# Optimization experiments

Measured on AMD Instinct MI355X. Metric: run time of the kernel, lower is better.

The kernel has to match this reference:

```python
import jax, jax.numpy as jnp
import numpy as np

MODEL_DIM = 1024
N_Q_HEADS = 16
N_GROUPS = 4
KV_PER_Q = N_Q_HEADS // N_GROUPS        # 4
HEAD_DIM = MODEL_DIM // N_Q_HEADS       # 64
KV_HEAD_DIM = MODEL_DIM // KV_PER_Q     # 256 (per-group K/V total width = N_GROUPS*HEAD_DIM)
ROPE_THETA = 50000.0


def rope_cos_sin(seq_len, dim, dtype):
    # standard RoPE tables: [S, dim]
    inv_freq = 1.0 / (ROPE_THETA ** (jnp.arange(0, dim, 2, dtype=jnp.float32) / dim))
    freqs = jnp.arange(seq_len, dtype=jnp.float32)[:, None] * inv_freq[None, :]  # [S, dim/2]
    emb = jnp.concatenate([freqs, freqs], axis=-1)                               # [S, dim]
    return jnp.cos(emb).astype(dtype), jnp.sin(emb).astype(dtype)


def rotate_half(x):
    h = x.shape[-1] // 2
    return jnp.concatenate([-x[..., h:], x[..., :h]], axis=-1)


def setup_inputs() -> dict:
    key = jax.random.key(0)
    k0, k1, k2, k3, k4 = jax.random.split(key, 5)
    B, S = 2, 2048
    qkv_out = MODEL_DIM + 2 * KV_HEAD_DIM  # 1536
    s_in = 1.0 / np.sqrt(MODEL_DIM)
    return {
        "x": jax.random.normal(k0, (B, S, MODEL_DIM), jnp.float32),
        "W_qkv": jax.random.normal(k1, (MODEL_DIM, qkv_out), jnp.float32) * s_in,
        "b_qkv": jnp.zeros((qkv_out,), jnp.float32),
        "W_out": jax.random.normal(k2, (MODEL_DIM, MODEL_DIM), jnp.float32) * s_in,
        "b_out": jnp.zeros((MODEL_DIM,), jnp.float32),
    }


def reference(x, W_qkv, b_qkv, W_out, b_out):
    B, S, _ = x.shape
    fused = x @ W_qkv + b_qkv  # [B,S,MODEL_DIM + 2*KV_HEAD_DIM]
    q, k, v = jnp.split(fused, [MODEL_DIM, MODEL_DIM + KV_HEAD_DIM], axis=-1)

    # [B,S,(NH HD)] -> [B,NH,S,HD]
    q = q.reshape(B, S, N_Q_HEADS, HEAD_DIM).transpose(0, 2, 1, 3)
    k = k.reshape(B, S, N_GROUPS, HEAD_DIM).transpose(0, 2, 1, 3)
    v = v.reshape(B, S, N_GROUPS, HEAD_DIM).transpose(0, 2, 1, 3)

    cos, sin = rope_cos_sin(S, HEAD_DIM, x.dtype)  # [S,HD]
    cos = cos[None, None]                          # [1,1,S,HD]
    sin = sin[None, None]
    q = q * cos + rotate_half(q) * sin
    k = k * cos + rotate_half(k) * sin

    # GQA without materializing duplicated heads: group queries [B,G,R,S,HD]
    qg = q.reshape(B, N_GROUPS, KV_PER_Q, S, HEAD_DIM)
    scale = 1.0 / np.sqrt(HEAD_DIM)
    scores = jnp.einsum('bgrsh,bgth->bgrst', qg, k) * scale  # [B,G,R,S,S]
    causal = jnp.tril(jnp.ones((S, S), bool))
    scores = jnp.where(causal, scores, jnp.finfo(scores.dtype).min)
    probs = jax.nn.softmax(scores, axis=-1)
    out = jnp.einsum('bgrst,bgth->bgrsh', probs, v)          # [B,G,R,S,HD]

    # [B,G,R,S,HD] -> [B,S,MODEL_DIM]  (head index = g*R + r, matching duplicate_heads)
    out = out.reshape(B, N_Q_HEADS, S, HEAD_DIM).transpose(0, 2, 1, 3).reshape(B, S, MODEL_DIM)
    return out @ W_out + b_out
```

## Files before the change

### kernel.cpp

```cpp
#include <hip/hip_runtime.h>
#include <hip/hip_bf16.h>

typedef __attribute__((ext_vector_type(8))) short short8;
typedef __attribute__((ext_vector_type(4))) float f32x4;

__device__ __forceinline__ short tobf(float f) {
  __hip_bfloat16 h = __float2bfloat16(f);
  return *reinterpret_cast<short*>(&h);
}
__device__ __forceinline__ float frombf(short s) {
  unsigned u = ((unsigned)(unsigned short)s) << 16;
  return __uint_as_float(u);
}

__device__ __forceinline__ int swz(int row) { return (row ^ (row >> 3)) & 7; }

#define GLDS16(gp, lp) __builtin_amdgcn_global_load_lds( \
    (__attribute__((address_space(1))) void*)(gp),       \
    (__attribute__((address_space(3))) void*)(lp), 16, 0, 0)

#define QSCALE 0.18033688011112042f

__global__ __launch_bounds__(256) void prep_k(
    const float* __restrict__ x, short* __restrict__ xb,
    const float* __restrict__ Wqkv, short* __restrict__ WqkvT,
    const float* __restrict__ Wout, short* __restrict__ WoutT,
    float* __restrict__ cost, float* __restrict__ sint) {
  __shared__ float t[64][65];
  const int bx = blockIdx.x, tid = threadIdx.x;
  if (bx < 1024) {
    int base = bx * 4096 + tid * 4;
#pragma unroll
    for (int rep = 0; rep < 4; ++rep) {
      int i = base + rep * 1024;
      float4 v = *(const float4*)(x + i);
      *(short4*)(xb + i) = make_short4(tobf(v.x), tobf(v.y), tobf(v.z), tobf(v.w));
    }
  } else if (bx < 1664) {
    const float* in;
    short* out;
    int C, bb;
    if (bx < 1408) { in = Wqkv; out = WqkvT; C = 1536; bb = bx - 1024; }
    else           { in = Wout; out = WoutT; C = 1024; bb = bx - 1408; }
    const int R = 1024;
    int nc = C >> 6;
    int br = bb / nc, bc = bb % nc;
    int lr = tid >> 6, lc = tid & 63;
#pragma unroll
    for (int j = 0; j < 16; ++j) {
      int r = j * 4 + lr;
      t[r][lc] = in[(size_t)(br * 64 + r) * C + bc * 64 + lc];
    }
    __syncthreads();
#pragma unroll
    for (int j = 0; j < 16; ++j) {
      int r = j * 4 + lr;
      out[(size_t)(bc * 64 + r) * R + br * 64 + lc] = tobf(t[lc][r]);
    }
  } else {
    int t2 = (bx - 1664) * 256 + tid;
    int s = t2 >> 5, f = t2 & 31;
    float inv = __expf(-(float)f * (logf(50000.0f) / 32.0f));
    float a = (float)s * inv;
    cost[t2] = cosf(a);
    sint[t2] = sinf(a);
  }
}

template <int MODE>
__global__ __launch_bounds__(256) void gemm_k(
    const short* __restrict__ A, const short* __restrict__ Bt,
    const float* __restrict__ bias, void* __restrict__ Cout,
    short* __restrict__ vT,
    int M, int N, int K,
    const float* __restrict__ cost, const float* __restrict__ sint) {
  __shared__ short As[128 * 64];
  __shared__ short Bs[64 * 64];
  const int ntile = N >> 6;
  const int bm = blockIdx.x / ntile, bn = blockIdx.x % ntile;
  const int tid = threadIdx.x, w = tid >> 6, l = tid & 63;
  const int c = l & 15, g = l >> 4;
  const int m0 = bm * 128, n0 = bn * 64;

  f32x4 acc[2][4] = {};

  for (int k0 = 0; k0 < K; k0 += 64) {
#pragma unroll
    for (int j = 0; j < 4; ++j) {
      int rb = j * 32 + w * 8;
      int row = rb + (l >> 3);
      int colel = ((l & 7) ^ swz(row)) * 8;
      GLDS16(A + (size_t)(m0 + row) * K + k0 + colel, &As[rb * 64]);
      if (j < 2) GLDS16(Bt + (size_t)(n0 + row) * K + k0 + colel, &Bs[rb * 64]);
    }
    __syncthreads();
#pragma unroll
    for (int kk = 0; kk < 2; ++kk) {
      short8 af[2], bf[4];
#pragma unroll
      for (int mi = 0; mi < 2; ++mi) {
        int row = w * 32 + mi * 16 + c;
        af[mi] = *(const short8*)&As[row * 64 + ((kk * 4 + g) ^ swz(row)) * 8];
      }
#pragma unroll
      for (int ni = 0; ni < 4; ++ni) {
        int row = ni * 16 + c;
        bf[ni] = *(const short8*)&Bs[row * 64 + ((kk * 4 + g) ^ swz(row)) * 8];
      }
#pragma unroll
      for (int mi = 0; mi < 2; ++mi)
#pragma unroll
        for (int ni = 0; ni < 4; ++ni)
          acc[mi][ni] = __builtin_amdgcn_mfma_f32_16x16x32_bf16(af[mi], bf[ni], acc[mi][ni], 0, 0, 0);
    }
    __syncthreads();
  }

  if (MODE == 0 && n0 >= 1280) {
    const int hg = (n0 - 1280) >> 6;
#pragma unroll
    for (int mi = 0; mi < 2; ++mi) {
      int m0r = m0 + w * 32 + mi * 16 + g * 4;
      int b = m0r >> 11, s = m0r & 2047;
#pragma unroll
      for (int ni = 0; ni < 4; ++ni) {
        int d = ni * 16 + c;
        float bs = bias[n0 + d];
        short4 o;
        o.x = tobf(acc[mi][ni][0] + bs);
        o.y = tobf(acc[mi][ni][1] + bs);
        o.z = tobf(acc[mi][ni][2] + bs);
        o.w = tobf(acc[mi][ni][3] + bs);
        *(short4*)&vT[(size_t)((b * 4 + hg) * 64 + d) * 2048 + s] = o;
      }
    }
    return;
  }

#pragma unroll
  for (int mi = 0; mi < 2; ++mi)
#pragma unroll
    for (int r = 0; r < 4; ++r) {
      int m = m0 + w * 32 + mi * 16 + g * 4 + r;
      int s = m & 2047;
#pragma unroll
      for (int ni = 0; ni < 4; ++ni) {
        int n = n0 + ni * 16 + c;
        float v = acc[mi][ni][r] + bias[n];
        if (MODE == 0) {
          int d = n & 63, f = d & 31;
          float cs = cost[s * 32 + f], sn = sint[s * 32 + f];
          float partner = acc[mi][ni ^ 2][r] + bias[n ^ 32];
          v = (d < 32) ? (v * cs - partner * sn) : (v * cs + partner * sn);
          if (n < 1024) v *= QSCALE;
          ((short*)Cout)[(size_t)m * N + n] = tobf(v);
        } else {
          ((float*)Cout)[(size_t)m * N + n] = v;
        }
      }
    }
}

__global__ __launch_bounds__(256) void attn_k(const short* __restrict__ qkv,
                                              const short* __restrict__ vT,
                                              short* __restrict__ pacc,
                                              float* __restrict__ plrun) {
  __shared__ short Ks2[2][64 * 64];
  __shared__ short Vt2[2][64 * 64];
  __shared__ short Ps[4][16 * 64];

  const int bx = blockIdx.x;
  const int bh = bx & 31;
  const int rest = bx >> 5;
  const int p = rest & 7;
  const int ci = rest >> 3;
  const int qtB = 15 - p, qtA = p;
  const int sB = 32 - 2 * p;
  const int start = (ci < 2) ? ci * 9 : 18 + (ci - 2) * 8;
  const int end = (ci < 2) ? start + 9 : start + 8;
  const int b = bh >> 4, h = bh & 15, hg = h >> 2;
  const int tid = threadIdx.x, w = tid >> 6, l = tid & 63;
  const int c = l & 15, g = l >> 4;
  const size_t rowbase = (size_t)(b * 2048) * 1536;

  const int i0row = w * 16 + (l >> 3);
  const int i1row = w * 16 + 8 + (l >> 3);
  const int c0 = ((l & 7) ^ swz(i0row)) * 8;
  const int c1 = ((l & 7) ^ swz(i1row)) * 8;
  const size_t k0off = (size_t)i0row * 1536 + c0;
  const size_t k1off = (size_t)i1row * 1536 + c1;
  const size_t v0off = (size_t)i0row * 2048 + c0;
  const size_t v1off = (size_t)i1row * 2048 + c1;
  const int lds0 = (w * 16) * 64;
  const int lds1 = (w * 16 + 8) * 64;
  const short* kbase = qkv + rowbase + 1024 + hg * 64;
  const short* vbase_p = vT + (size_t)((b * 4 + hg) * 64) * 2048;

#define KTOF(i) (((i) < sB) ? (i) : ((i) - sB))

  {
    int kt0 = KTOF(start);
    GLDS16(kbase + (size_t)kt0 * 98304 + k0off, &Ks2[0][lds0]);
    GLDS16(kbase + (size_t)kt0 * 98304 + k1off, &Ks2[0][lds1]);
    GLDS16(vbase_p + kt0 * 64 + v0off, &Vt2[0][lds0]);
    GLDS16(vbase_p + kt0 * 64 + v1off, &Vt2[0][lds1]);
  }
  asm volatile("s_waitcnt vmcnt(0)" ::: "memory");
  __builtin_amdgcn_s_barrier();
  __builtin_amdgcn_sched_barrier(0);

  f32x4 acco[2][4] = {};
  float lrun[2] = {0.f, 0.f};
  short* Pw = &Ps[w][0];
  short8 aq[2][2];

#pragma unroll
  for (int set = 0; set < 2; ++set)
#pragma unroll
    for (int kk = 0; kk < 2; ++kk)
      aq[set][kk] = *(const short8*)(qkv + rowbase +
          (size_t)(qtB * 128 + w * 32 + set * 16 + c) * 1536 + h * 64 + kk * 32 + g * 8);

#define BODY(qtc)                                                               \
  {                                                                             \
    const int cur = (i - start) & 1, nxt = cur ^ 1;                             \
    const int kt = KTOF(i);                                                     \
    if (i + 1 < end) {                         \
      int kt2 = KTOF(i + 1);                                                    \
      GLDS16(kbase + (size_t)kt2 * 98304 + k0off, &Ks2[nxt][lds0]);             \
      GLDS16(kbase + (size_t)kt2 * 98304 + k1off, &Ks2[nxt][lds1]);             \
      GLDS16(vbase_p + kt2 * 64 + v0off, &Vt2[nxt][lds0]);                      \
      GLDS16(vbase_p + kt2 * 64 + v1off, &Vt2[nxt][lds1]);                      \
    }                                                                           \
    short8 bk[2][4];                                                            \
    _Pragma("unroll") for (int kk = 0; kk < 2; ++kk)                            \
      _Pragma("unroll") for (int nb = 0; nb < 4; ++nb) {                        \
        int row = nb * 16 + c;                                                  \
        bk[kk][nb] = *(const short8*)&Ks2[cur][row * 64 + ((kk * 4 + g) ^ swz(row)) * 8]; \
      }                                                                         \
    f32x4 sfr[2][4] = {};                                                       \
    __builtin_amdgcn_s_setprio(1);                                              \
    _Pragma("unroll") for (int set = 0; set < 2; ++set)                         \
      _Pragma("unroll") for (int kk = 0; kk < 2; ++kk)                          \
        _Pragma("unroll") for (int nb = 0; nb < 4; ++nb)                        \
          sfr[set][nb] = __builtin_amdgcn_mfma_f32_16x16x32_bf16(               \
              bk[kk][nb], aq[set][kk], sfr[set][nb], 0, 0, 0);                  \
    __builtin_amdgcn_s_setprio(0);                                              \
    short8 bv[2][4];                                                            \
    _Pragma("unroll") for (int kk = 0; kk < 2; ++kk)                            \
      _Pragma("unroll") for (int nb = 0; nb < 4; ++nb) {                        \
        int row = nb * 16 + c;                                                  \
        bv[kk][nb] = *(const short8*)&Vt2[cur][row * 64 + ((kk * 4 + g) ^ swz(row)) * 8]; \
      }                                                                         \
    if (kt >= 2 * (qtc)) {            \
      _Pragma("unroll") for (int set = 0; set < 2; ++set) {                     \
        int qg = (qtc)*128 + w * 32 + set * 16 + c;                             \
        _Pragma("unroll") for (int nb = 0; nb < 4; ++nb)                        \
          _Pragma("unroll") for (int r = 0; r < 4; ++r)                         \
            if (kt * 64 + nb * 16 + g * 4 + r > qg) sfr[set][nb][r] = -1e30f;   \
      }                                                                         \
    }                                                                           \
    _Pragma("unroll") for (int set = 0; set < 2; ++set) {                       \
      float rs = 0.f;                                                           \
      _Pragma("unroll") for (int nb = 0; nb < 4; ++nb)                          \
        _Pragma("unroll") for (int r = 0; r < 4; ++r) {                         \
          float pv_ = exp2f(sfr[set][nb][r]);                                   \
          sfr[set][nb][r] = pv_;                                                \
          rs += pv_;                                                            \
        }                                                                       \
      rs += __shfl_xor(rs, 16, 64);                                             \
      rs += __shfl_xor(rs, 32, 64);                                             \
      lrun[set] += rs;                                                          \
      _Pragma("unroll") for (int nb = 0; nb < 4; ++nb) {                        \
        short4 pq;                                                              \
        pq.x = tobf(sfr[set][nb][0]);                                           \
        pq.y = tobf(sfr[set][nb][1]);                                           \
        pq.z = tobf(sfr[set][nb][2]);                                           \
        pq.w = tobf(sfr[set][nb][3]);                                           \
        int pslot = (nb * 2 + (g >> 1)) ^ swz(c);                               \
        *(short4*)&Pw[c * 64 + pslot * 8 + (g & 1) * 4] = pq;                   \
      }                                                                         \
      __builtin_amdgcn_s_setprio(1);                                            \
      _Pragma("unroll") for (int kk = 0; kk < 2; ++kk) {                        \
        short8 ap = *(const short8*)&Pw[c * 64 + (((kk * 4 + g) ^ swz(c)) * 8)];\
        _Pragma("unroll") for (int nb = 0; nb < 4; ++nb)                        \
          acco[set][nb] = __builtin_amdgcn_mfma_f32_16x16x32_bf16(              \
              ap, bv[kk][nb], acco[set][nb], 0, 0, 0);                          \
      }                                                                         \
      __builtin_amdgcn_s_setprio(0);                                            \
    }                                                                           \
    asm volatile("s_waitcnt vmcnt(0)" ::: "memory");                            \
    __builtin_amdgcn_s_barrier();                                               \
    __builtin_amdgcn_sched_barrier(0);                                          \
  }

#define STORE_PARTIAL(slot)                                                     \
  {                                                                             \
    size_t pb = ((size_t)(((bh * 8 + p) * 4 + ci) * 2 + (slot))) * 8192;        \
    int lb = (((bh * 8 + p) * 4 + ci) * 2 + (slot)) * 128;                      \
    _Pragma("unroll") for (int set = 0; set < 2; ++set) {                       \
      _Pragma("unroll") for (int nb = 0; nb < 4; ++nb)                          \
        _Pragma("unroll") for (int r = 0; r < 4; ++r) {                         \
          int row = w * 32 + set * 16 + g * 4 + r;                              \
          pacc[pb + row * 64 + nb * 16 + c] = tobf(acco[set][nb][r]);           \
          acco[set][nb][r] = 0.f;                                               \
        }                                                                       \
      if (g == 0) plrun[lb + w * 32 + set * 16 + c] = lrun[set];                \
      lrun[set] = 0.f;                                                          \
    }                                                                           \
  }

  int i = start;
  const int endB = (end < sB) ? end : sB;
  for (; i < endB; ++i) BODY(qtB);
  STORE_PARTIAL(0);

#pragma unroll
  for (int set = 0; set < 2; ++set)
#pragma unroll
    for (int kk = 0; kk < 2; ++kk)
      aq[set][kk] = *(const short8*)(qkv + rowbase +
          (size_t)(qtA * 128 + w * 32 + set * 16 + c) * 1536 + h * 64 + kk * 32 + g * 8);

  for (; i < end; ++i) BODY(qtA);
  STORE_PARTIAL(1);

#undef BODY
#undef STORE_PARTIAL
#undef KTOF
}

__global__ __launch_bounds__(256) void combine_k(const short* __restrict__ pacc,
                                                 const float* __restrict__ plrun,
                                                 short* __restrict__ attnb) {
  int e = blockIdx.x * 256 + threadIdx.x;
  int d8 = e & 7;
  int t = e >> 3;
  int row = t & 127;
  int t2 = t >> 7;
  int qt = t2 & 15;
  int bh = t2 >> 4;
  int p = (qt < 15 - qt) ? qt : 15 - qt;
  int slot = (qt >= 8) ? 0 : 1;
  float acc[8] = {};
  float lsum = 0.f;
#pragma unroll
  for (int ci = 0; ci < 4; ++ci) {
    int sidx = ((bh * 8 + p) * 4 + ci) * 2 + slot;
    short8 a = *(const short8*)(pacc + (size_t)sidx * 8192 + row * 64 + d8 * 8);
#pragma unroll
    for (int k = 0; k < 8; ++k) acc[k] += frombf(a[k]);
    lsum += plrun[sidx * 128 + row];
  }
  float li = 1.0f / lsum;
  int b = bh >> 4, h = bh & 15;
  int m = b * 2048 + qt * 128 + row;
  int n = h * 64 + d8 * 8;
  short8 o;
#pragma unroll
  for (int k = 0; k < 8; ++k) o[k] = tobf(acc[k] * li);
  *(short8*)(attnb + (size_t)m * 1024 + n) = o;
}

extern "C" void kernel_launch(void* const* d_in, const int* in_sizes, int n_in,
                              void* d_out, int out_size, void* d_ws, size_t ws_size,
                              hipStream_t stream) {
  const float* x    = (const float*)d_in[0];
  const float* Wqkv = (const float*)d_in[1];
  const float* bqkv = (const float*)d_in[2];
  const float* Wout = (const float*)d_in[3];
  const float* bout = (const float*)d_in[4];

  char* ws = (char*)d_ws;
  short* pacc  = (short*)(ws + 0);
  short* xb    = (short*)(ws + 0);
  short* WqkvT = (short*)(ws + 8388608);
  float* cost  = (float*)(ws + 11534336);
  float* sint  = (float*)(ws + 11796480);
  short* WoutT = (short*)(ws + 33554432);
  short* qkvb  = (short*)(ws + 35651584);
  short* attnb = (short*)(ws + 35651584);
  short* vTb   = (short*)(ws + 48234496);
  float* plrun = (float*)(ws + 50331648);

  prep_k<<<1920, 256, 0, stream>>>(x, xb, Wqkv, WqkvT, Wout, WoutT, cost, sint);
  gemm_k<0><<<768, 256, 0, stream>>>(xb, WqkvT, bqkv, (void*)qkvb, vTb, 4096, 1536, 1024, cost, sint);
  attn_k<<<1024, 256, 0, stream>>>(qkvb, vTb, pacc, plrun);
  combine_k<<<2048, 256, 0, stream>>>(pacc, plrun, attnb);
  gemm_k<1><<<512, 256, 0, stream>>>(attnb, WoutT, bout, d_out, nullptr, 4096, 1024, 1024, cost, sint);
}
```

Before: 106.6 us.

## Use 256-row query tiles, 512-thread blocks and triple-buffered K/V prefetch in attention

The attention kernel now processes 256-query-row tiles with 8 waves per block instead of 128 rows with 4 waves. Each K/V tile loaded to LDS is therefore shared by twice as many query rows. The causal work split changes from four chunks per query-pair to two halves of 18 tiles each, so there are fewer partials for the combine step to merge. K/V loads move to a 3-stage ring buffer with prefetch distance 2 and partial vmcnt waits, to hide more global-load latency. The cost is 256 blocks instead of 1024, which may underfill the 256 CUs and leave less parallelism across the grid.

```diff
diff --git a/kernel.cpp b/kernel.cpp
--- a/kernel.cpp
+++ b/kernel.cpp
@@ -161,51 +161,46 @@
     }
 }
 
-__global__ __launch_bounds__(256) void attn_k(const short* __restrict__ qkv,
+__global__ __launch_bounds__(512) void attn_k(const short* __restrict__ qkv,
                                               const short* __restrict__ vT,
                                               short* __restrict__ pacc,
                                               float* __restrict__ plrun) {
-  __shared__ short Ks2[2][64 * 64];
-  __shared__ short Vt2[2][64 * 64];
-  __shared__ short Ps[4][16 * 64];
+  __shared__ short Ks3[3][64 * 64];
+  __shared__ short Vt3[3][64 * 64];
+  __shared__ short Ps[8][16 * 64];
 
   const int bx = blockIdx.x;
   const int bh = bx & 31;
   const int rest = bx >> 5;
-  const int p = rest & 7;
-  const int ci = rest >> 3;
-  const int qtB = 15 - p, qtA = p;
-  const int sB = 32 - 2 * p;
-  const int start = (ci < 2) ? ci * 9 : 18 + (ci - 2) * 8;
-  const int end = (ci < 2) ? start + 9 : start + 8;
+  const int p = rest & 3;
+  const int half = rest >> 2;
+  const int qtB = 7 - p, qtA = p;
+  const int sB = 32 - 4 * p;
+  const int start = half * 18;
+  const int end = start + 18;
   const int b = bh >> 4, h = bh & 15, hg = h >> 2;
   const int tid = threadIdx.x, w = tid >> 6, l = tid & 63;
   const int c = l & 15, g = l >> 4;
   const size_t rowbase = (size_t)(b * 2048) * 1536;
 
-  const int i0row = w * 16 + (l >> 3);
-  const int i1row = w * 16 + 8 + (l >> 3);
-  const int c0 = ((l & 7) ^ swz(i0row)) * 8;
-  const int c1 = ((l & 7) ^ swz(i1row)) * 8;
-  const size_t k0off = (size_t)i0row * 1536 + c0;
-  const size_t k1off = (size_t)i1row * 1536 + c1;
-  const size_t v0off = (size_t)i0row * 2048 + c0;
-  const size_t v1off = (size_t)i1row * 2048 + c1;
-  const int lds0 = (w * 16) * 64;
-  const int lds1 = (w * 16 + 8) * 64;
+  const int srow = w * 8 + (l >> 3);
+  const int scol = ((l & 7) ^ swz(srow)) * 8;
+  const size_t koff = (size_t)srow * 1536 + scol;
+  const size_t voff = (size_t)srow * 2048 + scol;
+  const int ldsoff = (w * 8) * 64;
   const short* kbase = qkv + rowbase + 1024 + hg * 64;
   const short* vbase_p = vT + (size_t)((b * 4 + hg) * 64) * 2048;
 
 #define KTOF(i) (((i) < sB) ? (i) : ((i) - sB))
 
   {
-    int kt0 = KTOF(start);
-    GLDS16(kbase + (size_t)kt0 * 98304 + k0off, &Ks2[0][lds0]);
-    GLDS16(kbase + (size_t)kt0 * 98304 + k1off, &Ks2[0][lds1]);
-    GLDS16(vbase_p + kt0 * 64 + v0off, &Vt2[0][lds0]);
-    GLDS16(vbase_p + kt0 * 64 + v1off, &Vt2[0][lds1]);
-  }
-  asm volatile("s_waitcnt vmcnt(0)" ::: "memory");
+    int t0 = KTOF(start), t1 = KTOF(start + 1);
+    GLDS16(kbase + (size_t)t0 * 98304 + koff, &Ks3[0][ldsoff]);
+    GLDS16(vbase_p + t0 * 64 + voff, &Vt3[0][ldsoff]);
+    GLDS16(kbase + (size_t)t1 * 98304 + koff, &Ks3[1][ldsoff]);
+    GLDS16(vbase_p + t1 * 64 + voff, &Vt3[1][ldsoff]);
+  }
+  asm volatile("s_waitcnt vmcnt(2)" ::: "memory");
   __builtin_amdgcn_s_barrier();
   __builtin_amdgcn_sched_barrier(0);
 
@@ -213,30 +208,29 @@
   float lrun[2] = {0.f, 0.f};
   short* Pw = &Ps[w][0];
   short8 aq[2][2];
+  int cur = 0, s2 = 2;
 
 #pragma unroll
   for (int set = 0; set < 2; ++set)
 #pragma unroll
     for (int kk = 0; kk < 2; ++kk)
       aq[set][kk] = *(const short8*)(qkv + rowbase +
-          (size_t)(qtB * 128 + w * 32 + set * 16 + c) * 1536 + h * 64 + kk * 32 + g * 8);
+          (size_t)(qtB * 256 + w * 32 + set * 16 + c) * 1536 + h * 64 + kk * 32 + g * 8);
 
 #define BODY(qtc)                                                               \
   {                                                                             \
-    const int cur = (i - start) & 1, nxt = cur ^ 1;                             \
     const int kt = KTOF(i);                                                     \
-    if (i + 1 < end) {                         \
-      int kt2 = KTOF(i + 1);                                                    \
-      GLDS16(kbase + (size_t)kt2 * 98304 + k0off, &Ks2[nxt][lds0]);             \
-      GLDS16(kbase + (size_t)kt2 * 98304 + k1off, &Ks2[nxt][lds1]);             \
-      GLDS16(vbase_p + kt2 * 64 + v0off, &Vt2[nxt][lds0]);                      \
-      GLDS16(vbase_p + kt2 * 64 + v1off, &Vt2[nxt][lds1]);                      \
+    const bool pf2 = (i + 2 < end);                                             \
+    if (pf2) {         \
+      int ktp = KTOF(i + 2);                                                    \
+      GLDS16(kbase + (size_t)ktp * 98304 + koff, &Ks3[s2][ldsoff]);             \
+      GLDS16(vbase_p + ktp * 64 + voff, &Vt3[s2][ldsoff]);                      \
     }                                                                           \
     short8 bk[2][4];                                                            \
     _Pragma("unroll") for (int kk = 0; kk < 2; ++kk)                            \
       _Pragma("unroll") for (int nb = 0; nb < 4; ++nb) {                        \
         int row = nb * 16 + c;                                                  \
-        bk[kk][nb] = *(const short8*)&Ks2[cur][row * 64 + ((kk * 4 + g) ^ swz(row)) * 8]; \
+        bk[kk][nb] = *(const short8*)&Ks3[cur][row * 64 + ((kk * 4 + g) ^ swz(row)) * 8]; \
       }                                                                         \
     f32x4 sfr[2][4] = {};                                                       \
     __builtin_amdgcn_s_setprio(1);                                              \
@@ -250,11 +244,11 @@
     _Pragma("unroll") for (int kk = 0; kk < 2; ++kk)                            \
       _Pragma("unroll") for (int nb = 0; nb < 4; ++nb) {                        \
         int row = nb * 16 + c;                                                  \
-        bv[kk][nb] = *(const short8*)&Vt2[cur][row * 64 + ((kk * 4 + g) ^ swz(row)) * 8]; \
-      }                                                                         \
-    if (kt >= 2 * (qtc)) {            \
+        bv[kk][nb] = *(const short8*)&Vt3[cur][row * 64 + ((kk * 4 + g) ^ swz(row)) * 8]; \
+      }                                                                         \
+    if (kt >= 4 * (qtc)) {            \
       _Pragma("unroll") for (int set = 0; set < 2; ++set) {                     \
-        int qg = (qtc)*128 + w * 32 + set * 16 + c;                             \
+        int qg = (qtc)*256 + w * 32 + set * 16 + c;                             \
         _Pragma("unroll") for (int nb = 0; nb < 4; ++nb)                        \
           _Pragma("unroll") for (int r = 0; r < 4; ++r)                         \
             if (kt * 64 + nb * 16 + g * 4 + r > qg) sfr[set][nb][r] = -1e30f;   \
@@ -289,15 +283,18 @@
       }                                                                         \
       __builtin_amdgcn_s_setprio(0);                                            \
     }                                                                           \
-    asm volatile("s_waitcnt vmcnt(0)" ::: "memory");                            \
+    if (pf2) asm volatile("s_waitcnt vmcnt(2)" ::: "memory");                   \
+    else     asm volatile("s_waitcnt vmcnt(0)" ::: "memory");                   \
     __builtin_amdgcn_s_barrier();                                               \
     __builtin_amdgcn_sched_barrier(0);                                          \
+    cur = (cur == 2) ? 0 : cur + 1;                                             \
+    s2 = (s2 == 2) ? 0 : s2 + 1;                                                \
   }
 
 #define STORE_PARTIAL(slot)                                                     \
   {                                                                             \
-    size_t pb = ((size_t)(((bh * 8 + p) * 4 + ci) * 2 + (slot))) * 8192;        \
-    int lb = (((bh * 8 + p) * 4 + ci) * 2 + (slot)) * 128;                      \
+    int sidx = ((bh * 4 + p) * 2 + half) * 2 + (slot);                          \
+    size_t pb = (size_t)sidx * 16384;                                           \
     _Pragma("unroll") for (int set = 0; set < 2; ++set) {                       \
       _Pragma("unroll") for (int nb = 0; nb < 4; ++nb)                          \
         _Pragma("unroll") for (int r = 0; r < 4; ++r) {                         \
@@ -305,7 +302,7 @@
           pacc[pb + row * 64 + nb * 16 + c] = tobf(acco[set][nb][r]);           \
           acco[set][nb][r] = 0.f;                                               \
         }                                                                       \
-      if (g == 0) plrun[lb + w * 32 + set * 16 + c] = lrun[set];                \
+      if (g == 0) plrun[sidx * 256 + w * 32 + set * 16 + c] = lrun[set];        \
       lrun[set] = 0.f;                                                          \
     }                                                                           \
   }
@@ -320,7 +317,7 @@
 #pragma unroll
     for (int kk = 0; kk < 2; ++kk)
       aq[set][kk] = *(const short8*)(qkv + rowbase +
-          (size_t)(qtA * 128 + w * 32 + set * 16 + c) * 1536 + h * 64 + kk * 32 + g * 8);
+          (size_t)(qtA * 256 + w * 32 + set * 16 + c) * 1536 + h * 64 + kk * 32 + g * 8);
 
   for (; i < end; ++i) BODY(qtA);
   STORE_PARTIAL(1);
@@ -336,25 +333,25 @@
   int e = blockIdx.x * 256 + threadIdx.x;
   int d8 = e & 7;
   int t = e >> 3;
-  int row = t & 127;
-  int t2 = t >> 7;
-  int qt = t2 & 15;
-  int bh = t2 >> 4;
-  int p = (qt < 15 - qt) ? qt : 15 - qt;
-  int slot = (qt >= 8) ? 0 : 1;
+  int row = t & 255;
+  int t2 = t >> 8;
+  int qt = t2 & 7;
+  int bh = t2 >> 3;
+  int p = (qt < 7 - qt) ? qt : 7 - qt;
+  int slot = (qt >= 4) ? 0 : 1;
   float acc[8] = {};
   float lsum = 0.f;
 #pragma unroll
-  for (int ci = 0; ci < 4; ++ci) {
-    int sidx = ((bh * 8 + p) * 4 + ci) * 2 + slot;
-    short8 a = *(const short8*)(pacc + (size_t)sidx * 8192 + row * 64 + d8 * 8);
+  for (int half = 0; half < 2; ++half) {
+    int sidx = ((bh * 4 + p) * 2 + half) * 2 + slot;
+    short8 a = *(const short8*)(pacc + (size_t)sidx * 16384 + row * 64 + d8 * 8);
 #pragma unroll
     for (int k = 0; k < 8; ++k) acc[k] += frombf(a[k]);
-    lsum += plrun[sidx * 128 + row];
+    lsum += plrun[sidx * 256 + row];
   }
   float li = 1.0f / lsum;
   int b = bh >> 4, h = bh & 15;
-  int m = b * 2048 + qt * 128 + row;
+  int m = b * 2048 + qt * 256 + row;
   int n = h * 64 + d8 * 8;
   short8 o;
 #pragma unroll
@@ -385,7 +382,7 @@
 
   prep_k<<<1920, 256, 0, stream>>>(x, xb, Wqkv, WqkvT, Wout, WoutT, cost, sint);
   gemm_k<0><<<768, 256, 0, stream>>>(xb, WqkvT, bqkv, (void*)qkvb, vTb, 4096, 1536, 1024, cost, sint);
-  attn_k<<<1024, 256, 0, stream>>>(qkvb, vTb, pacc, plrun);
+  attn_k<<<256, 512, 0, stream>>>(qkvb, vTb, pacc, plrun);
   combine_k<<<2048, 256, 0, stream>>>(pacc, plrun, attnb);
   gemm_k<1><<<512, 256, 0, stream>>>(attnb, WoutT, bout, d_out, nullptr, 4096, 1024, 1024, cost, sint);
 }
```

Result: faster. 99.91 us (-6.3%).
